# Optimization experiments

Hardware: AMD Instinct MI355X
Metric: run time of the kernel (lower is better)

Reference implementation:

```python
import jax, jax.numpy as jnp
import numpy as np

N = 50000       # nodes
E = 800000      # directed edges (before self-loops)
IN_C = 128
HID = 32
HEADS = 4
OUT_C = 64
NEG_SLOPE = 0.2  # PyG GATConv default leaky relu slope


def setup_inputs() -> dict:
    key = jax.random.key(0)
    ks = jax.random.split(key, 11)
    x = jax.random.normal(ks[0], (N, IN_C), jnp.float32)
    edge_index = jax.random.randint(ks[1], (2, E), 0, N, dtype=jnp.int32)
    # conv1: in -> HEADS*HID, concat=True
    W1 = jax.random.normal(ks[2], (IN_C, HEADS * HID), jnp.float32) / np.sqrt(IN_C)
    att_src1 = jax.random.normal(ks[3], (HEADS, HID), jnp.float32) / np.sqrt(HID)
    att_dst1 = jax.random.normal(ks[4], (HEADS, HID), jnp.float32) / np.sqrt(HID)
    b1 = jnp.zeros((HEADS * HID,), jnp.float32)
    # conv2: HEADS*HID -> OUT_C, heads=1, concat=False
    W2 = jax.random.normal(ks[5], (HEADS * HID, OUT_C), jnp.float32) / np.sqrt(HEADS * HID)
    att_src2 = jax.random.normal(ks[6], (1, OUT_C), jnp.float32) / np.sqrt(OUT_C)
    att_dst2 = jax.random.normal(ks[7], (1, OUT_C), jnp.float32) / np.sqrt(OUT_C)
    b2 = jnp.zeros((OUT_C,), jnp.float32)
    return dict(x=x, edge_index=edge_index, W1=W1, att_src1=att_src1,
                att_dst1=att_dst1, b1=b1, W2=W2, att_src2=att_src2,
                att_dst2=att_dst2, b2=b2)


def _gat_conv(x, src, dst, W, att_src, att_dst, bias, heads, ch, concat):
    # x: [N, F_in]; src/dst: [E'] (self-loops already included)
    h = (x @ W).reshape(N, heads, ch)                 # [N, H, C]
    a_s = jnp.sum(h * att_src[None], axis=-1)         # [N, H]
    a_d = jnp.sum(h * att_dst[None], axis=-1)         # [N, H]
    e = jax.nn.leaky_relu(a_s[src] + a_d[dst], NEG_SLOPE)  # [E', H]
    # numerically-stable edge softmax over destination neighborhoods
    m = jax.ops.segment_max(e, dst, num_segments=N)   # [N, H]
    m = jnp.where(jnp.isfinite(m), m, 0.0)
    ee = jnp.exp(e - jax.lax.stop_gradient(m)[dst])
    denom = jax.ops.segment_sum(ee, dst, num_segments=N)  # [N, H]
    alpha = ee / (denom[dst] + 1e-16)                 # [E', H]
    msg = h[src] * alpha[:, :, None]                  # [E', H, C]
    out = jax.ops.segment_sum(msg, dst, num_segments=N)   # [N, H, C]
    if concat:
        out = out.reshape(N, heads * ch)
    else:
        out = out.mean(axis=1)
    return out + bias


def reference(x, edge_index, W1, att_src1, att_dst1, b1, W2, att_src2, att_dst2, b2):
    # PyG GATConv adds self-loops by default
    loop = jnp.arange(N, dtype=edge_index.dtype)
    src = jnp.concatenate([edge_index[0], loop])
    dst = jnp.concatenate([edge_index[1], loop])
    # dropout layers are identity in eval mode (training=False)
    h = _gat_conv(x, src, dst, W1, att_src1, att_dst1, b1, HEADS, HID, True)
    h = jax.nn.elu(h)
    out = _gat_conv(h, src, dst, W2, att_src2, att_dst2, b2, 1, OUT_C, False)
    return out
```

## Files before the change

kernel.cpp:

```cpp
#include <hip/hip_runtime.h>
#include <math.h>

namespace {
constexpr int N_   = 50000;
constexpr int E_   = 800000;
constexpr int EP_  = E_ + N_;
constexpr float SLOPE = 0.2f;

constexpr int NB_    = (N_ + 127) / 128;
constexpr int CHUNK_ = 8192;
constexpr int NBLKA_ = (EP_ + CHUNK_ - 1) / CHUNK_;
constexpr int CAPB_  = 4096;
constexpr int NBLKG_ = (N_ + 63) / 64;

constexpr size_t OFF_H1  = 0;
constexpr size_t OFF_Y1  = OFF_H1  + (size_t)N_ * 128 * 2;
constexpr size_t OFF_H2  = OFF_Y1  + (size_t)N_ * 128 * 2;
constexpr size_t OFF_AS1 = OFF_H2  + (size_t)N_ * 64 * 2;
constexpr size_t OFF_AD1 = OFF_AS1 + (size_t)N_ * 4 * 4;
constexpr size_t OFF_AS2 = OFF_AD1 + (size_t)N_ * 4 * 4;
constexpr size_t OFF_AD2 = OFF_AS2 + (size_t)N_ * 4;
constexpr size_t OFF_ROW = OFF_AD2 + (size_t)N_ * 4;
constexpr size_t OFF_GC  = OFF_ROW + (((size_t)(N_ + 1) * 4 + 15) & ~(size_t)15);
constexpr size_t OFF_GO  = OFF_GC  + (((size_t)NB_ * 4 + 15) & ~(size_t)15);
constexpr size_t OFF_GU  = OFF_GO  + (((size_t)(NB_ + 1) * 4 + 15) & ~(size_t)15);
constexpr size_t OFF_EB1 = OFF_GU  + (((size_t)NB_ * 4 + 15) & ~(size_t)15);
constexpr size_t OFF_EB  = OFF_EB1 + (size_t)EP_ * 4;
}

typedef __attribute__((ext_vector_type(8))) short short8;
typedef __attribute__((ext_vector_type(4))) float f32x4;

__device__ __forceinline__ unsigned short f2bf(float x) {
  unsigned u = __float_as_uint(x);
  return (unsigned short)((u + 0x7FFFu + ((u >> 16) & 1u)) >> 16);
}
__device__ __forceinline__ unsigned pack2bf(float a, float b) {
  return (unsigned)f2bf(a) | ((unsigned)f2bf(b) << 16);
}
__device__ __forceinline__ float bf_lo(unsigned u) { return __uint_as_float(u << 16); }
__device__ __forceinline__ float bf_hi(unsigned u) { return __uint_as_float(u & 0xFFFF0000u); }

__global__ __launch_bounds__(256, 3) void k_g1h(const float* __restrict__ x,
    const float* __restrict__ W, const float* __restrict__ av_s,
    const float* __restrict__ av_d, unsigned short* __restrict__ hbf,
    float* __restrict__ a_s, float* __restrict__ a_d,
    const int* __restrict__ ei, int* __restrict__ gcount)
{
  __shared__ __align__(16) char smem[52224];
  const int t = threadIdx.x;
  if (blockIdx.x >= NBLKG_) {
    int* nh = (int*)smem;
    for (int j = t; j < NB_; j += 256) nh[j] = 0;
    __syncthreads();
    const int beg = (blockIdx.x - NBLKG_) * CHUNK_;
    const int end = min(beg + CHUNK_, EP_);
    for (int i = beg + t; i < end; i += 256) {
      const int dd = (i < E_) ? ei[E_ + i] : (i - E_);
      atomicAdd(&nh[dd >> 7], 1);
    }
    __syncthreads();
    for (int j = t; j < NB_; j += 256)
      if (nh[j]) atomicAdd(&gcount[j], nh[j]);
    return;
  }
  unsigned short* xs = (unsigned short*)smem;
  unsigned*       wt = (unsigned*)(smem + 17408);
  float*         wtf = (float*)(smem + 17408);
  const int rbase = blockIdx.x * 64;
#pragma unroll
  for (int it = 0; it < 8; ++it) {
    const int fidx = t + it * 256;
    const int row = fidx >> 5;
    const int c4  = fidx & 31;
    const int rg  = rbase + row;
    float4 v = (rg < N_) ? ((const float4*)x)[(size_t)rg * 32 + c4]
                         : make_float4(0.f, 0.f, 0.f, 0.f);
    *(uint2*)&xs[row * 136 + c4 * 4] =
        make_uint2(pack2bf(v.x, v.y), pack2bf(v.z, v.w));
  }
#pragma unroll
  for (int it = 0; it < 32; ++it) {
    const int idx = t + it * 256;
    const int n  = idx & 127;
    const int kk = idx >> 7;
    wt[n * 68 + kk] = pack2bf(W[(2 * kk) * 128 + n], W[(2 * kk + 1) * 128 + n]);
  }
  __syncthreads();
  const int wv = t >> 6;
  const int l  = t & 63;
  const int lr = l & 15;
  const int lg = l >> 4;
  f32x4 acc[8];
#pragma unroll
  for (int j = 0; j < 8; ++j) acc[j] = (f32x4){0.f, 0.f, 0.f, 0.f};
#pragma unroll
  for (int ks = 0; ks < 4; ++ks) {
    const short8 a = *(const short8*)&xs[(wv * 16 + lr) * 136 + ks * 32 + lg * 8];
#pragma unroll
    for (int j = 0; j < 8; ++j) {
      const short8 b = *(const short8*)&wt[(j * 16 + lr) * 68 + ks * 16 + lg * 4];
      acc[j] = __builtin_amdgcn_mfma_f32_16x16x32_bf16(a, b, acc[j], 0, 0, 0);
    }
  }
  __syncthreads();
#pragma unroll
  for (int j = 0; j < 8; ++j)
#pragma unroll
    for (int r = 0; r < 4; ++r)
      wtf[(wv * 16 + lg * 4 + r) * 132 + j * 16 + lr] = acc[j][r];
  __syncthreads();
#pragma unroll
  for (int it = 0; it < 16; ++it) {
    const int idx = t + it * 256;
    const int row = idx >> 6;
    const int c2  = idx & 63;
    const int rg  = rbase + row;
    if (rg < N_) {
      const float2 hv = *(const float2*)&wtf[row * 132 + c2 * 2];
      ((unsigned*)hbf)[(size_t)rg * 64 + c2] = pack2bf(hv.x, hv.y);
    }
  }
  {
    const int row = t & 63;
    const int q   = t >> 6;
    const int rg  = rbase + row;
    float ss = 0.f, sd = 0.f;
#pragma unroll
    for (int i = 0; i < 8; ++i) {
      const float4 hv = *(const float4*)&wtf[row * 132 + q * 32 + 4 * i];
      const float4 s4 = *(const float4*)&av_s[q * 32 + 4 * i];
      const float4 d4 = *(const float4*)&av_d[q * 32 + 4 * i];
      ss += hv.x * s4.x + hv.y * s4.y + hv.z * s4.z + hv.w * s4.w;
      sd += hv.x * d4.x + hv.y * d4.y + hv.z * d4.z + hv.w * d4.w;
    }
    if (rg < N_) { a_s[rg * 4 + q] = ss; a_d[rg * 4 + q] = sd; }
  }
}

__global__ __launch_bounds__(256, 4) void k_gemm2(const unsigned* __restrict__ ybf,
    const float* __restrict__ W, const float* __restrict__ av_s,
    const float* __restrict__ av_d, unsigned short* __restrict__ hbf,
    float* __restrict__ a_s, float* __restrict__ a_d)
{
  __shared__ __align__(16) char smem[36864];
  unsigned short* xs = (unsigned short*)smem;
  unsigned*       wt = (unsigned*)(smem + 17408);
  float*         wtf = (float*)(smem + 17408);
  float*          ps = (float*)(smem + 34816);
  const int t = threadIdx.x;
  const int rbase = blockIdx.x * 64;
#pragma unroll
  for (int it = 0; it < 16; ++it) {
    const int idx = t + it * 256;
    const int row = idx >> 6;
    const int c2  = idx & 63;
    const int rg  = rbase + row;
    const unsigned u = (rg < N_) ? ybf[(size_t)rg * 64 + c2] : 0u;
    *(unsigned*)&xs[row * 136 + c2 * 2] = u;
  }
#pragma unroll
  for (int it = 0; it < 16; ++it) {
    const int idx = t + it * 256;
    const int n  = idx & 63;
    const int kk = idx >> 6;
    wt[n * 68 + kk] = pack2bf(W[(2 * kk) * 64 + n], W[(2 * kk + 1) * 64 + n]);
  }
  __syncthreads();
  const int wv = t >> 6;
  const int l  = t & 63;
  const int lr = l & 15;
  const int lg = l >> 4;
  f32x4 acc[4];
#pragma unroll
  for (int j = 0; j < 4; ++j) acc[j] = (f32x4){0.f, 0.f, 0.f, 0.f};
#pragma unroll
  for (int ks = 0; ks < 4; ++ks) {
    const short8 a = *(const short8*)&xs[(wv * 16 + lr) * 136 + ks * 32 + lg * 8];
#pragma unroll
    for (int j = 0; j < 4; ++j) {
      const short8 b = *(const short8*)&wt[(j * 16 + lr) * 68 + ks * 16 + lg * 4];
      acc[j] = __builtin_amdgcn_mfma_f32_16x16x32_bf16(a, b, acc[j], 0, 0, 0);
    }
  }
  __syncthreads();
#pragma unroll
  for (int j = 0; j < 4; ++j)
#pragma unroll
    for (int r = 0; r < 4; ++r)
      wtf[(wv * 16 + lg * 4 + r) * 68 + j * 16 + lr] = acc[j][r];
  __syncthreads();
#pragma unroll
  for (int it = 0; it < 8; ++it) {
    const int idx = t + it * 256;
    const int row = idx >> 5;
    const int c2  = idx & 31;
    const int rg  = rbase + row;
    if (rg < N_) {
      const float2 hv = *(const float2*)&wtf[row * 68 + c2 * 2];
      ((unsigned*)hbf)[(size_t)rg * 32 + c2] = pack2bf(hv.x, hv.y);
    }
  }
  {
    const int row = t & 63;
    const int g   = t >> 6;
    float ss = 0.f, sd = 0.f;
#pragma unroll
    for (int i = 0; i < 4; ++i) {
      const float4 hv = *(const float4*)&wtf[row * 68 + g * 16 + 4 * i];
      const float4 s4 = *(const float4*)&av_s[g * 16 + 4 * i];
      const float4 d4 = *(const float4*)&av_d[g * 16 + 4 * i];
      ss += hv.x * s4.x + hv.y * s4.y + hv.z * s4.z + hv.w * s4.w;
      sd += hv.x * d4.x + hv.y * d4.y + hv.z * d4.z + hv.w * d4.w;
    }
    ps[g * 64 + row] = ss;
    ps[256 + g * 64 + row] = sd;
  }
  __syncthreads();
  if (t < 64) {
    const int rg = rbase + t;
    if (rg < N_) {
      a_s[rg] = ps[t] + ps[64 + t] + ps[128 + t] + ps[192 + t];
      a_d[rg] = ps[256 + t] + ps[320 + t] + ps[384 + t] + ps[448 + t];
    }
  }
}

__global__ __launch_bounds__(512) void k_scan(const int* __restrict__ gcount,
    int* __restrict__ goff, int* __restrict__ gcursor)
{
  __shared__ int sd[512];
  const int t = threadIdx.x;
  const int v = (t < NB_) ? gcount[t] : 0;
  sd[t] = v;
  __syncthreads();
  for (int off = 1; off < 512; off <<= 1) {
    const int add = (t >= off) ? sd[t - off] : 0;
    __syncthreads();
    sd[t] += add;
    __syncthreads();
  }
  if (t < NB_) { goff[t] = sd[t] - v; gcursor[t] = sd[t] - v; }
  if (t == 0) goff[NB_] = EP_;
}

__global__ __launch_bounds__(256) void k_scatter(const int* __restrict__ ei,
    int* __restrict__ gcursor, unsigned* __restrict__ eb1)
{
  __shared__ int nh[NB_];
  __shared__ int gb[NB_];
  const int t = threadIdx.x;
  for (int j = t; j < NB_; j += 256) nh[j] = 0;
  __syncthreads();
  const int beg = blockIdx.x * CHUNK_;
  const int end = min(beg + CHUNK_, EP_);
  for (int i = beg + t; i < end; i += 256) {
    const int d = (i < E_) ? ei[E_ + i] : (i - E_);
    atomicAdd(&nh[d >> 7], 1);
  }
  __syncthreads();
  for (int j = t; j < NB_; j += 256) {
    const int c = nh[j];
    gb[j] = c ? atomicAdd(&gcursor[j], c) : 0;
    nh[j] = 0;
  }
  __syncthreads();
  for (int i = beg + t; i < end; i += 256) {
    int s, d;
    if (i < E_) { s = ei[i]; d = ei[E_ + i]; } else { s = d = i - E_; }
    const int b = d >> 7;
    const int r = atomicAdd(&nh[b], 1);
    eb1[gb[b] + r] = ((unsigned)s << 16) | (unsigned)d;
  }
}

__global__ __launch_bounds__(256) void k_bucket(const unsigned* __restrict__ eb1,
    const int* __restrict__ goff, int* __restrict__ rowptr,
    int* __restrict__ ebuf)
{
  __shared__ int h[128];
  __shared__ int off[129];
  __shared__ unsigned arrv[CAPB_];
  const int b = blockIdx.x;
  const int t = threadIdx.x;
  const int base = goff[b];
  const int cnt  = goff[b + 1] - base;
  if (t < 128) h[t] = 0;
  __syncthreads();
  const bool fits = (cnt <= CAPB_);
  for (int i = t; i < cnt; i += 256) {
    const unsigned v = eb1[base + i];
    if (fits) arrv[i] = v;
    atomicAdd(&h[(int)(v & 0xFFFFu) - (b << 7)], 1);
  }
  __syncthreads();
  if (t < 64) {
    const int a0 = h[2 * t], a1 = h[2 * t + 1];
    int s = a0 + a1;
#pragma unroll
    for (int m = 1; m < 64; m <<= 1) {
      const int u = __shfl_up(s, m);
      if (t >= m) s += u;
    }
    off[2 * t + 1] = s - a1;
    off[2 * t]     = s - a1 - a0;
    if (t == 63) off[128] = s;
  }
  __syncthreads();
  if (t < 128) {
    const int dst = (b << 7) + t;
    if (dst < N_) rowptr[dst] = base + off[t];
  }
  if (b == NB_ - 1 && t == 0) rowptr[N_] = EP_;
  if (t < 128) h[t] = 0;
  __syncthreads();
  for (int i = t; i < cnt; i += 256) {
    const unsigned v = fits ? arrv[i] : eb1[base + i];
    const int dlow = (int)(v & 0xFFFFu) - (b << 7);
    const int r = atomicAdd(&h[dlow], 1);
    ebuf[base + off[dlow] + r] = (int)(v >> 16);
  }
}

__global__ __launch_bounds__(256, 4) void k_agg1(const int* __restrict__ rowptr,
    const int* __restrict__ ebuf, const float* __restrict__ a_s,
    const float* __restrict__ a_d, const unsigned short* __restrict__ hbf,
    const float* __restrict__ b1, unsigned* __restrict__ y)
{
  __shared__ uint2 pl[4][4 * 65];
  const int w = threadIdx.x >> 6;
  const int l = threadIdx.x & 63;
  const int d = blockIdx.x * 2 + (w >> 1);
  const int half = w & 1;
  const int base = rowptr[d];
  const int deg  = rowptr[d + 1] - base;
  const float4 ad = *(const float4*)&a_d[(size_t)d * 4];
  const int pe = l >> 5;
  const int ci = half * 32 + (l & 31);
  const int hsel = ci >> 4;
  const unsigned ci4 = (unsigned)ci * 4u;
  float acc0 = 0.f, acc1 = 0.f;
  float r0, r1, r2, r3;

  if (deg <= 64) {
    int   sreg = 0;
    float e0 = -1e30f, e1 = -1e30f, e2 = -1e30f, e3 = -1e30f;
    if (l < deg) {
      sreg = ebuf[base + l];
      const float4 as = *(const float4*)&a_s[(size_t)sreg * 4];
      e0 = as.x + ad.x; e0 = e0 > 0.f ? e0 : SLOPE * e0;
      e1 = as.y + ad.y; e1 = e1 > 0.f ? e1 : SLOPE * e1;
      e2 = as.z + ad.z; e2 = e2 > 0.f ? e2 : SLOPE * e2;
      e3 = as.w + ad.w; e3 = e3 > 0.f ? e3 : SLOPE * e3;
    }
    float mx0 = e0, mx1 = e1, mx2 = e2, mx3 = e3;
#pragma unroll
    for (int m = 32; m >= 1; m >>= 1) {
      mx0 = fmaxf(mx0, __shfl_xor(mx0, m));
      mx1 = fmaxf(mx1, __shfl_xor(mx1, m));
      mx2 = fmaxf(mx2, __shfl_xor(mx2, m));
      mx3 = fmaxf(mx3, __shfl_xor(mx3, m));
    }
    const float p0 = (l < deg) ? __expf(e0 - mx0) : 0.f;
    const float p1 = (l < deg) ? __expf(e1 - mx1) : 0.f;
    const float p2 = (l < deg) ? __expf(e2 - mx2) : 0.f;
    const float p3 = (l < deg) ? __expf(e3 - mx3) : 0.f;
    float sm0 = p0, sm1 = p1, sm2 = p2, sm3 = p3;
#pragma unroll
    for (int m = 32; m >= 1; m >>= 1) {
      sm0 += __shfl_xor(sm0, m);
      sm1 += __shfl_xor(sm1, m);
      sm2 += __shfl_xor(sm2, m);
      sm3 += __shfl_xor(sm3, m);
    }
    r0 = 1.f / (sm0 + 1e-16f);
    r1 = 1.f / (sm1 + 1e-16f);
    r2 = 1.f / (sm2 + 1e-16f);
    r3 = 1.f / (sm3 + 1e-16f);
    {
      const unsigned soff = (unsigned)sreg << 8;
      pl[w][0 * 65 + l] = make_uint2(soff, __float_as_uint(p0));
      pl[w][1 * 65 + l] = make_uint2(soff, __float_as_uint(p1));
      pl[w][2 * 65 + l] = make_uint2(soff, __float_as_uint(p2));
      pl[w][3 * 65 + l] = make_uint2(soff, __float_as_uint(p3));
    }
    const uint2* __restrict__ rp = &pl[w][hsel * 65 + pe];
    const int niter = (deg + 15) >> 4;
    int it = 0;
    for (; it + 2 <= niter; it += 2) {
      unsigned uA[8], uB[8];
      float pA[8], pB[8];
#pragma unroll
      for (int u = 0; u < 8; ++u) {
        const uint2 sp = rp[it * 16 + 2 * u];
        pA[u] = __uint_as_float(sp.y);
        uA[u] = *(const unsigned*)((const char*)hbf + (sp.x + ci4));
      }
#pragma unroll
      for (int u = 0; u < 8; ++u) {
        const uint2 sp = rp[it * 16 + 16 + 2 * u];
        pB[u] = __uint_as_float(sp.y);
        uB[u] = *(const unsigned*)((const char*)hbf + (sp.x + ci4));
      }
#pragma unroll
      for (int u = 0; u < 8; ++u) {
        acc0 = fmaf(pA[u], bf_lo(uA[u]), acc0);
        acc1 = fmaf(pA[u], bf_hi(uA[u]), acc1);
      }
#pragma unroll
      for (int u = 0; u < 8; ++u) {
        acc0 = fmaf(pB[u], bf_lo(uB[u]), acc0);
        acc1 = fmaf(pB[u], bf_hi(uB[u]), acc1);
      }
    }
    if (it < niter) {
      unsigned uA[8];
      float pA[8];
#pragma unroll
      for (int u = 0; u < 8; ++u) {
        const uint2 sp = rp[it * 16 + 2 * u];
        pA[u] = __uint_as_float(sp.y);
        uA[u] = *(const unsigned*)((const char*)hbf + (sp.x + ci4));
      }
#pragma unroll
      for (int u = 0; u < 8; ++u) {
        acc0 = fmaf(pA[u], bf_lo(uA[u]), acc0);
        acc1 = fmaf(pA[u], bf_hi(uA[u]), acc1);
      }
    }
  } else {
    float mx0 = -1e30f, mx1 = -1e30f, mx2 = -1e30f, mx3 = -1e30f;
    for (int i = l; i < deg; i += 64) {
      const int s = ebuf[base + i];
      const float4 as = *(const float4*)&a_s[(size_t)s * 4];
      float e0 = as.x + ad.x; e0 = e0 > 0.f ? e0 : SLOPE * e0;
      float e1 = as.y + ad.y; e1 = e1 > 0.f ? e1 : SLOPE * e1;
      float e2 = as.z + ad.z; e2 = e2 > 0.f ? e2 : SLOPE * e2;
      float e3 = as.w + ad.w; e3 = e3 > 0.f ? e3 : SLOPE * e3;
      mx0 = fmaxf(mx0, e0); mx1 = fmaxf(mx1, e1);
      mx2 = fmaxf(mx2, e2); mx3 = fmaxf(mx3, e3);
    }
#pragma unroll
    for (int m = 32; m >= 1; m >>= 1) {
      mx0 = fmaxf(mx0, __shfl_xor(mx0, m));
      mx1 = fmaxf(mx1, __shfl_xor(mx1, m));
      mx2 = fmaxf(mx2, __shfl_xor(mx2, m));
      mx3 = fmaxf(mx3, __shfl_xor(mx3, m));
    }
    float sm0 = 0.f, sm1 = 0.f, sm2 = 0.f, sm3 = 0.f;
    for (int i = l; i < deg; i += 64) {
      const int s = ebuf[base + i];
      const float4 as = *(const float4*)&a_s[(size_t)s * 4];
      float e0 = as.x + ad.x; e0 = e0 > 0.f ? e0 : SLOPE * e0;
      float e1 = as.y + ad.y; e1 = e1 > 0.f ? e1 : SLOPE * e1;
      float e2 = as.z + ad.z; e2 = e2 > 0.f ? e2 : SLOPE * e2;
      float e3 = as.w + ad.w; e3 = e3 > 0.f ? e3 : SLOPE * e3;
      sm0 += __expf(e0 - mx0); sm1 += __expf(e1 - mx1);
      sm2 += __expf(e2 - mx2); sm3 += __expf(e3 - mx3);
    }
#pragma unroll
    for (int m = 32; m >= 1; m >>= 1) {
      sm0 += __shfl_xor(sm0, m);
      sm1 += __shfl_xor(sm1, m);
      sm2 += __shfl_xor(sm2, m);
      sm3 += __shfl_xor(sm3, m);
    }
    r0 = 1.f / (sm0 + 1e-16f);
    r1 = 1.f / (sm1 + 1e-16f);
    r2 = 1.f / (sm2 + 1e-16f);
    r3 = 1.f / (sm3 + 1e-16f);
    const float mxs = hsel == 3 ? mx3 : hsel == 2 ? mx2 : hsel == 1 ? mx1 : mx0;
    for (int i = 0; i < deg; i += 2) {
      const int e = i + pe;
      if (e < deg) {
        const int s = ebuf[base + e];
        const float4 as = *(const float4*)&a_s[(size_t)s * 4];
        float e0 = as.x + ad.x; e0 = e0 > 0.f ? e0 : SLOPE * e0;
        float e1 = as.y + ad.y; e1 = e1 > 0.f ? e1 : SLOPE * e1;
        float e2 = as.z + ad.z; e2 = e2 > 0.f ? e2 : SLOPE * e2;
        float e3 = as.w + ad.w; e3 = e3 > 0.f ? e3 : SLOPE * e3;
        const float es = hsel == 3 ? e3 : hsel == 2 ? e2 : hsel == 1 ? e1 : e0;
        const float pa = __expf(es - mxs);
        const unsigned uu = ((const unsigned*)(hbf + (size_t)s * 128))[ci];
        acc0 = fmaf(pa, bf_lo(uu), acc0);
        acc1 = fmaf(pa, bf_hi(uu), acc1);
      }
    }
  }
  acc0 += __shfl_xor(acc0, 32);
  acc1 += __shfl_xor(acc1, 32);
  if (pe == 0) {
    const float rsel = hsel == 3 ? r3 : hsel == 2 ? r2 : hsel == 1 ? r1 : r0;
    const int c0 = 2 * ci;
    const float2 bb = *(const float2*)&b1[c0];
    float o0 = acc0 * rsel + bb.x;
    float o1 = acc1 * rsel + bb.y;
    o0 = o0 > 0.f ? o0 : expm1f(o0);
    o1 = o1 > 0.f ? o1 : expm1f(o1);
    y[(size_t)d * 64 + ci] = pack2bf(o0, o1);
  }
}

__global__ __launch_bounds__(256, 4) void k_agg2(const int* __restrict__ rowptr,
    const int* __restrict__ ebuf, const float* __restrict__ a_s,
    const float* __restrict__ a_d, const unsigned short* __restrict__ hbf,
    const float* __restrict__ b2, float* __restrict__ out)
{
  __shared__ uint2 pl2[4][66];
  const int w = threadIdx.x >> 6;
  const int l = threadIdx.x & 63;
  const int lh = l & 31;
  const bool hi = (l >= 32);
  const int d = blockIdx.x * 4 + w;
  const int base = rowptr[d];
  const int deg  = rowptr[d + 1] - base;
  const float ad = a_d[d];
  const unsigned lh4 = (unsigned)lh * 4u;
  float acc0 = 0.f, acc1 = 0.f;
  float rv;

  if (deg <= 64) {
    int   sreg = 0;
    float e = -1e30f;
    if (l < deg) {
      sreg = ebuf[base + l];
      e = a_s[sreg] + ad; e = e > 0.f ? e : SLOPE * e;
    }
    float mx = e;
#pragma unroll
    for (int m = 32; m >= 1; m >>= 1) mx = fmaxf(mx, __shfl_xor(mx, m));
    const float p = (l < deg) ? __expf(e - mx) : 0.f;
    float sm = p;
#pragma unroll
    for (int m = 32; m >= 1; m >>= 1) sm += __shfl_xor(sm, m);
    rv = 1.f / (sm + 1e-16f);
    pl2[w][l] = make_uint2((unsigned)(l < deg ? sreg : 0) << 7,
                           __float_as_uint(p));
    const uint2* __restrict__ rp = &pl2[w][hi ? 1 : 0];
    const int niter = (deg + 15) >> 4;
    int it = 0;
    for (; it + 2 <= niter; it += 2) {
      unsigned uA[8], uB[8];
      float pA[8], pB[8];
#pragma unroll
      for (int u = 0; u < 8; ++u) {
        const uint2 sp = rp[it * 16 + 2 * u];
        pA[u] = __uint_as_float(sp.y);
        uA[u] = *(const unsigned*)((const char*)hbf + (sp.x + lh4));
      }
#pragma unroll
      for (int u = 0; u < 8; ++u) {
        const uint2 sp = rp[it * 16 + 16 + 2 * u];
        pB[u] = __uint_as_float(sp.y);
        uB[u] = *(const unsigned*)((const char*)hbf + (sp.x + lh4));
      }
#pragma unroll
      for (int u = 0; u < 8; ++u) {
        acc0 = fmaf(pA[u], bf_lo(uA[u]), acc0);
        acc1 = fmaf(pA[u], bf_hi(uA[u]), acc1);
      }
#pragma unroll
      for (int u = 0; u < 8; ++u) {
        acc0 = fmaf(pB[u], bf_lo(uB[u]), acc0);
        acc1 = fmaf(pB[u], bf_hi(uB[u]), acc1);
      }
    }
    if (it < niter) {
      unsigned uA[8];
      float pA[8];
#pragma unroll
      for (int u = 0; u < 8; ++u) {
        const uint2 sp = rp[it * 16 + 2 * u];
        pA[u] = __uint_as_float(sp.y);
        uA[u] = *(const unsigned*)((const char*)hbf + (sp.x + lh4));
      }
#pragma unroll
      for (int u = 0; u < 8; ++u) {
        acc0 = fmaf(pA[u], bf_lo(uA[u]), acc0);
        acc1 = fmaf(pA[u], bf_hi(uA[u]), acc1);
      }
    }
  } else {
    float mx = -1e30f;
    for (int i = l; i < deg; i += 64) {
      const int s = ebuf[base + i];
      float e = a_s[s] + ad; e = e > 0.f ? e : SLOPE * e;
      mx = fmaxf(mx, e);
    }
#pragma unroll
    for (int m = 32; m >= 1; m >>= 1) mx = fmaxf(mx, __shfl_xor(mx, m));
    float sm = 0.f;
    for (int i = l; i < deg; i += 64) {
      const int s = ebuf[base + i];
      float e = a_s[s] + ad; e = e > 0.f ? e : SLOPE * e;
      sm += __expf(e - mx);
    }
#pragma unroll
    for (int m = 32; m >= 1; m >>= 1) sm += __shfl_xor(sm, m);
    rv = 1.f / (sm + 1e-16f);
    for (int i = 0; i < deg; ++i) {
      const int s = ebuf[base + i];
      float e = a_s[s] + ad; e = e > 0.f ? e : SLOPE * e;
      const float pp = hi ? 0.f : __expf(e - mx);
      const unsigned uu = ((const unsigned*)(hbf + (size_t)s * 64))[lh];
      acc0 = fmaf(pp, bf_lo(uu), acc0);
      acc1 = fmaf(pp, bf_hi(uu), acc1);
    }
  }
  acc0 += __shfl_xor(acc0, 32);
  acc1 += __shfl_xor(acc1, 32);
  if (!hi) {
    const int c0 = 2 * lh;
    const float2 bb = *(const float2*)&b2[c0];
    *(float2*)&out[(size_t)d * 64 + c0] =
        make_float2(acc0 * rv + bb.x, acc1 * rv + bb.y);
  }
}

extern "C" void kernel_launch(void* const* d_in, const int* in_sizes, int n_in,
                              void* d_out, int out_size, void* d_ws, size_t ws_size,
                              hipStream_t stream) {
  const float* x     = (const float*)d_in[0];
  const int*   ei    = (const int*)d_in[1];
  const float* W1    = (const float*)d_in[2];
  const float* as1v  = (const float*)d_in[3];
  const float* ad1v  = (const float*)d_in[4];
  const float* b1    = (const float*)d_in[5];
  const float* W2    = (const float*)d_in[6];
  const float* as2v  = (const float*)d_in[7];
  const float* ad2v  = (const float*)d_in[8];
  const float* b2    = (const float*)d_in[9];
  float* out = (float*)d_out;

  char* ws = (char*)d_ws;
  unsigned short* h1 = (unsigned short*)(ws + OFF_H1);
  unsigned* y1       = (unsigned*)(ws + OFF_Y1);
  unsigned short* h2 = (unsigned short*)(ws + OFF_H2);
  float* a_s1 = (float*)(ws + OFF_AS1);
  float* a_d1 = (float*)(ws + OFF_AD1);
  float* a_s2 = (float*)(ws + OFF_AS2);
  float* a_d2 = (float*)(ws + OFF_AD2);
  int* rowptr = (int*)(ws + OFF_ROW);
  int* gcount = (int*)(ws + OFF_GC);
  int* goff   = (int*)(ws + OFF_GO);
  int* gcur   = (int*)(ws + OFF_GU);
  unsigned* eb1 = (unsigned*)(ws + OFF_EB1);
  int* ebuf   = (int*)(ws + OFF_EB);

  hipMemsetAsync(gcount, 0, (size_t)NB_ * 4, stream);

  k_g1h<<<NBLKG_ + NBLKA_, 256, 0, stream>>>(x, W1, as1v, ad1v, h1, a_s1, a_d1,
                                             ei, gcount);
  k_scan<<<1, 512, 0, stream>>>(gcount, goff, gcur);
  k_scatter<<<NBLKA_, 256, 0, stream>>>(ei, gcur, eb1);
  k_bucket<<<NB_, 256, 0, stream>>>(eb1, goff, rowptr, ebuf);
  k_agg1<<<N_ / 2, 256, 0, stream>>>(rowptr, ebuf, a_s1, a_d1, h1, b1, y1);
  k_gemm2<<<NBLKG_, 256, 0, stream>>>(y1, W2, as2v, ad2v, h2, a_s2, a_d2);
  k_agg2<<<N_ / 4, 256, 0, stream>>>(rowptr, ebuf, a_s2, a_d2, h2, b2, out);
}
```

Baseline: 178.9 us.

## Map one wavefront per node in aggregation kernels with 8-byte bf16 gathers

k_agg1 now assigns one full wavefront per destination node instead of two wavefronts per node. Each lane gathers 4 bf16 channels (uint2) per neighbor, so two edge slots cover the 128-channel row. k_agg2 likewise uses uint2 gathers over 16 lanes with four edges in flight, finishing with two shuffle reductions. The aim is to halve duplicated softmax work and wave count in agg1 and widen memory transactions, at the cost of more registers and fewer lanes per node for the gather.

```diff
diff --git a/kernel.cpp b/kernel.cpp
--- a/kernel.cpp
+++ b/kernel.cpp
@@ -330,17 +330,10 @@
   __shared__ uint2 pl[4][4 * 65];
   const int w = threadIdx.x >> 6;
   const int l = threadIdx.x & 63;
-  const int d = blockIdx.x * 2 + (w >> 1);
-  const int half = w & 1;
+  const int d = blockIdx.x * 4 + w;
   const int base = rowptr[d];
   const int deg  = rowptr[d + 1] - base;
   const float4 ad = *(const float4*)&a_d[(size_t)d * 4];
-  const int pe = l >> 5;
-  const int ci = half * 32 + (l & 31);
-  const int hsel = ci >> 4;
-  const unsigned ci4 = (unsigned)ci * 4u;
-  float acc0 = 0.f, acc1 = 0.f;
-  float r0, r1, r2, r3;
 
   if (deg <= 64) {
     int   sreg = 0;
@@ -373,10 +366,10 @@
       sm2 += __shfl_xor(sm2, m);
       sm3 += __shfl_xor(sm3, m);
     }
-    r0 = 1.f / (sm0 + 1e-16f);
-    r1 = 1.f / (sm1 + 1e-16f);
-    r2 = 1.f / (sm2 + 1e-16f);
-    r3 = 1.f / (sm3 + 1e-16f);
+    const float r0 = 1.f / (sm0 + 1e-16f);
+    const float r1 = 1.f / (sm1 + 1e-16f);
+    const float r2 = 1.f / (sm2 + 1e-16f);
+    const float r3 = 1.f / (sm3 + 1e-16f);
     {
       const unsigned soff = (unsigned)sreg << 8;
       pl[w][0 * 65 + l] = make_uint2(soff, __float_as_uint(p0));
@@ -384,51 +377,81 @@
       pl[w][2 * 65 + l] = make_uint2(soff, __float_as_uint(p2));
       pl[w][3 * 65 + l] = make_uint2(soff, __float_as_uint(p3));
     }
-    const uint2* __restrict__ rp = &pl[w][hsel * 65 + pe];
+    const int eh = l >> 5;
+    const int cl = l & 31;
+    const int hsel = cl >> 3;
+    const unsigned coff = (unsigned)cl * 8u;
+    const uint2* __restrict__ rp = &pl[w][hsel * 65];
+    float acc0 = 0.f, acc1 = 0.f, acc2 = 0.f, acc3 = 0.f;
     const int niter = (deg + 15) >> 4;
-    int it = 0;
-    for (; it + 2 <= niter; it += 2) {
-      unsigned uA[8], uB[8];
+    int bt = 0;
+    for (; bt + 2 <= niter; bt += 2) {
+      uint2 uA[8], uB[8];
       float pA[8], pB[8];
 #pragma unroll
       for (int u = 0; u < 8; ++u) {
-        const uint2 sp = rp[it * 16 + 2 * u];
+        const uint2 sp = rp[bt * 16 + 2 * u + eh];
         pA[u] = __uint_as_float(sp.y);
-        uA[u] = *(const unsigned*)((const char*)hbf + (sp.x + ci4));
-      }
-#pragma unroll
-      for (int u = 0; u < 8; ++u) {
-        const uint2 sp = rp[it * 16 + 16 + 2 * u];
+        uA[u] = *(const uint2*)((const char*)hbf + (sp.x + coff));
+      }
+#pragma unroll
+      for (int u = 0; u < 8; ++u) {
+        const uint2 sp = rp[bt * 16 + 16 + 2 * u + eh];
         pB[u] = __uint_as_float(sp.y);
-        uB[u] = *(const unsigned*)((const char*)hbf + (sp.x + ci4));
-      }
-#pragma unroll
-      for (int u = 0; u < 8; ++u) {
-        acc0 = fmaf(pA[u], bf_lo(uA[u]), acc0);
-        acc1 = fmaf(pA[u], bf_hi(uA[u]), acc1);
-      }
-#pragma unroll
-      for (int u = 0; u < 8; ++u) {
-        acc0 = fmaf(pB[u], bf_lo(uB[u]), acc0);
-        acc1 = fmaf(pB[u], bf_hi(uB[u]), acc1);
-      }
-    }
-    if (it < niter) {
-      unsigned uA[8];
+        uB[u] = *(const uint2*)((const char*)hbf + (sp.x + coff));
+      }
+#pragma unroll
+      for (int u = 0; u < 8; ++u) {
+        acc0 = fmaf(pA[u], bf_lo(uA[u].x), acc0);
+        acc1 = fmaf(pA[u], bf_hi(uA[u].x), acc1);
+        acc2 = fmaf(pA[u], bf_lo(uA[u].y), acc2);
+        acc3 = fmaf(pA[u], bf_hi(uA[u].y), acc3);
+      }
+#pragma unroll
+      for (int u = 0; u < 8; ++u) {
+        acc0 = fmaf(pB[u], bf_lo(uB[u].x), acc0);
+        acc1 = fmaf(pB[u], bf_hi(uB[u].x), acc1);
+        acc2 = fmaf(pB[u], bf_lo(uB[u].y), acc2);
+        acc3 = fmaf(pB[u], bf_hi(uB[u].y), acc3);
+      }
+    }
+    if (bt < niter) {
+      uint2 uA[8];
       float pA[8];
 #pragma unroll
       for (int u = 0; u < 8; ++u) {
-        const uint2 sp = rp[it * 16 + 2 * u];
+        const uint2 sp = rp[bt * 16 + 2 * u + eh];
         pA[u] = __uint_as_float(sp.y);
-        uA[u] = *(const unsigned*)((const char*)hbf + (sp.x + ci4));
-      }
-#pragma unroll
-      for (int u = 0; u < 8; ++u) {
-        acc0 = fmaf(pA[u], bf_lo(uA[u]), acc0);
-        acc1 = fmaf(pA[u], bf_hi(uA[u]), acc1);
-      }
+        uA[u] = *(const uint2*)((const char*)hbf + (sp.x + coff));
+      }
+#pragma unroll
+      for (int u = 0; u < 8; ++u) {
+        acc0 = fmaf(pA[u], bf_lo(uA[u].x), acc0);
+        acc1 = fmaf(pA[u], bf_hi(uA[u].x), acc1);
+        acc2 = fmaf(pA[u], bf_lo(uA[u].y), acc2);
+        acc3 = fmaf(pA[u], bf_hi(uA[u].y), acc3);
+      }
+    }
+    acc0 += __shfl_xor(acc0, 32);
+    acc1 += __shfl_xor(acc1, 32);
+    acc2 += __shfl_xor(acc2, 32);
+    acc3 += __shfl_xor(acc3, 32);
+    if (eh == 0) {
+      const float rsel = hsel == 3 ? r3 : hsel == 2 ? r2 : hsel == 1 ? r1 : r0;
+      const float4 bb = *(const float4*)&b1[4 * cl];
+      float o0 = acc0 * rsel + bb.x;
+      float o1 = acc1 * rsel + bb.y;
+      float o2 = acc2 * rsel + bb.z;
+      float o3 = acc3 * rsel + bb.w;
+      o0 = o0 > 0.f ? o0 : expm1f(o0);
+      o1 = o1 > 0.f ? o1 : expm1f(o1);
+      o2 = o2 > 0.f ? o2 : expm1f(o2);
+      o3 = o3 > 0.f ? o3 : expm1f(o3);
+      *(uint2*)&y[(size_t)d * 64 + 2 * cl] =
+          make_uint2(pack2bf(o0, o1), pack2bf(o2, o3));
     }
   } else {
+    const int hsel = l >> 4;
     float mx0 = -1e30f, mx1 = -1e30f, mx2 = -1e30f, mx3 = -1e30f;
     for (int i = l; i < deg; i += 64) {
       const int s = ebuf[base + i];
@@ -465,39 +488,32 @@
       sm2 += __shfl_xor(sm2, m);
       sm3 += __shfl_xor(sm3, m);
     }
-    r0 = 1.f / (sm0 + 1e-16f);
-    r1 = 1.f / (sm1 + 1e-16f);
-    r2 = 1.f / (sm2 + 1e-16f);
-    r3 = 1.f / (sm3 + 1e-16f);
+    const float r0 = 1.f / (sm0 + 1e-16f);
+    const float r1 = 1.f / (sm1 + 1e-16f);
+    const float r2 = 1.f / (sm2 + 1e-16f);
+    const float r3 = 1.f / (sm3 + 1e-16f);
     const float mxs = hsel == 3 ? mx3 : hsel == 2 ? mx2 : hsel == 1 ? mx1 : mx0;
-    for (int i = 0; i < deg; i += 2) {
-      const int e = i + pe;
-      if (e < deg) {
-        const int s = ebuf[base + e];
-        const float4 as = *(const float4*)&a_s[(size_t)s * 4];
-        float e0 = as.x + ad.x; e0 = e0 > 0.f ? e0 : SLOPE * e0;
-        float e1 = as.y + ad.y; e1 = e1 > 0.f ? e1 : SLOPE * e1;
-        float e2 = as.z + ad.z; e2 = e2 > 0.f ? e2 : SLOPE * e2;
-        float e3 = as.w + ad.w; e3 = e3 > 0.f ? e3 : SLOPE * e3;
-        const float es = hsel == 3 ? e3 : hsel == 2 ? e2 : hsel == 1 ? e1 : e0;
-        const float pa = __expf(es - mxs);
-        const unsigned uu = ((const unsigned*)(hbf + (size_t)s * 128))[ci];
-        acc0 = fmaf(pa, bf_lo(uu), acc0);
-        acc1 = fmaf(pa, bf_hi(uu), acc1);
-      }
-    }
-  }
-  acc0 += __shfl_xor(acc0, 32);
-  acc1 += __shfl_xor(acc1, 32);
-  if (pe == 0) {
+    float acc0 = 0.f, acc1 = 0.f;
+    for (int i = 0; i < deg; ++i) {
+      const int s = ebuf[base + i];
+      const float4 as = *(const float4*)&a_s[(size_t)s * 4];
+      float e0 = as.x + ad.x; e0 = e0 > 0.f ? e0 : SLOPE * e0;
+      float e1 = as.y + ad.y; e1 = e1 > 0.f ? e1 : SLOPE * e1;
+      float e2 = as.z + ad.z; e2 = e2 > 0.f ? e2 : SLOPE * e2;
+      float e3 = as.w + ad.w; e3 = e3 > 0.f ? e3 : SLOPE * e3;
+      const float es = hsel == 3 ? e3 : hsel == 2 ? e2 : hsel == 1 ? e1 : e0;
+      const float pa = __expf(es - mxs);
+      const unsigned uu = ((const unsigned*)(hbf + (size_t)s * 128))[l];
+      acc0 = fmaf(pa, bf_lo(uu), acc0);
+      acc1 = fmaf(pa, bf_hi(uu), acc1);
+    }
     const float rsel = hsel == 3 ? r3 : hsel == 2 ? r2 : hsel == 1 ? r1 : r0;
-    const int c0 = 2 * ci;
-    const float2 bb = *(const float2*)&b1[c0];
+    const float2 bb = *(const float2*)&b1[2 * l];
     float o0 = acc0 * rsel + bb.x;
     float o1 = acc1 * rsel + bb.y;
     o0 = o0 > 0.f ? o0 : expm1f(o0);
     o1 = o1 > 0.f ? o1 : expm1f(o1);
-    y[(size_t)d * 64 + ci] = pack2bf(o0, o1);
+    y[(size_t)d * 64 + l] = pack2bf(o0, o1);
   }
 }
 
@@ -509,15 +525,10 @@
   __shared__ uint2 pl2[4][66];
   const int w = threadIdx.x >> 6;
   const int l = threadIdx.x & 63;
-  const int lh = l & 31;
-  const bool hi = (l >= 32);
   const int d = blockIdx.x * 4 + w;
   const int base = rowptr[d];
   const int deg  = rowptr[d + 1] - base;
   const float ad = a_d[d];
-  const unsigned lh4 = (unsigned)lh * 4u;
-  float acc0 = 0.f, acc1 = 0.f;
-  float rv;
 
   if (deg <= 64) {
     int   sreg = 0;
@@ -533,54 +544,80 @@
     float sm = p;
 #pragma unroll
     for (int m = 32; m >= 1; m >>= 1) sm += __shfl_xor(sm, m);
-    rv = 1.f / (sm + 1e-16f);
+    const float rv = 1.f / (sm + 1e-16f);
     pl2[w][l] = make_uint2((unsigned)(l < deg ? sreg : 0) << 7,
                            __float_as_uint(p));
-    const uint2* __restrict__ rp = &pl2[w][hi ? 1 : 0];
-    const int niter = (deg + 15) >> 4;
-    int it = 0;
-    for (; it + 2 <= niter; it += 2) {
-      unsigned uA[8], uB[8];
+    const int eq = l >> 4;
+    const int cl = l & 15;
+    const unsigned coff = (unsigned)cl * 8u;
+    const uint2* __restrict__ rp = &pl2[w][0];
+    float acc0 = 0.f, acc1 = 0.f, acc2 = 0.f, acc3 = 0.f;
+    const int niter = (deg + 31) >> 5;
+    int bt = 0;
+    for (; bt + 2 <= niter; bt += 2) {
+      uint2 uA[8], uB[8];
       float pA[8], pB[8];
 #pragma unroll
       for (int u = 0; u < 8; ++u) {
-        const uint2 sp = rp[it * 16 + 2 * u];
+        const uint2 sp = rp[bt * 32 + 4 * u + eq];
         pA[u] = __uint_as_float(sp.y);
-        uA[u] = *(const unsigned*)((const char*)hbf + (sp.x + lh4));
-      }
-#pragma unroll
-      for (int u = 0; u < 8; ++u) {
-        const uint2 sp = rp[it * 16 + 16 + 2 * u];
+        uA[u] = *(const uint2*)((const char*)hbf + (sp.x + coff));
+      }
+#pragma unroll
+      for (int u = 0; u < 8; ++u) {
+        const uint2 sp = rp[bt * 32 + 32 + 4 * u + eq];
         pB[u] = __uint_as_float(sp.y);
-        uB[u] = *(const unsigned*)((const char*)hbf + (sp.x + lh4));
-      }
-#pragma unroll
-      for (int u = 0; u < 8; ++u) {
-        acc0 = fmaf(pA[u], bf_lo(uA[u]), acc0);
-        acc1 = fmaf(pA[u], bf_hi(uA[u]), acc1);
-      }
-#pragma unroll
-      for (int u = 0; u < 8; ++u) {
-        acc0 = fmaf(pB[u], bf_lo(uB[u]), acc0);
-        acc1 = fmaf(pB[u], bf_hi(uB[u]), acc1);
-      }
-    }
-    if (it < niter) {
-      unsigned uA[8];
+        uB[u] = *(const uint2*)((const char*)hbf + (sp.x + coff));
+      }
+#pragma unroll
+      for (int u = 0; u < 8; ++u) {
+        acc0 = fmaf(pA[u], bf_lo(uA[u].x), acc0);
+        acc1 = fmaf(pA[u], bf_hi(uA[u].x), acc1);
+        acc2 = fmaf(pA[u], bf_lo(uA[u].y), acc2);
+        acc3 = fmaf(pA[u], bf_hi(uA[u].y), acc3);
+      }
+#pragma unroll
+      for (int u = 0; u < 8; ++u) {
+        acc0 = fmaf(pB[u], bf_lo(uB[u].x), acc0);
+        acc1 = fmaf(pB[u], bf_hi(uB[u].x), acc1);
+        acc2 = fmaf(pB[u], bf_lo(uB[u].y), acc2);
+        acc3 = fmaf(pB[u], bf_hi(uB[u].y), acc3);
+      }
+    }
+    if (bt < niter) {
+      uint2 uA[8];
       float pA[8];
 #pragma unroll
       for (int u = 0; u < 8; ++u) {
-        const uint2 sp = rp[it * 16 + 2 * u];
+        const uint2 sp = rp[bt * 32 + 4 * u + eq];
         pA[u] = __uint_as_float(sp.y);
-        uA[u] = *(const unsigned*)((const char*)hbf + (sp.x + lh4));
-      }
-#pragma unroll
-      for (int u = 0; u < 8; ++u) {
-        acc0 = fmaf(pA[u], bf_lo(uA[u]), acc0);
-        acc1 = fmaf(pA[u], bf_hi(uA[u]), acc1);
-      }
+        uA[u] = *(const uint2*)((const char*)hbf + (sp.x + coff));
+      }
+#pragma unroll
+      for (int u = 0; u < 8; ++u) {
+        acc0 = fmaf(pA[u], bf_lo(uA[u].x), acc0);
+        acc1 = fmaf(pA[u], bf_hi(uA[u].x), acc1);
+        acc2 = fmaf(pA[u], bf_lo(uA[u].y), acc2);
+        acc3 = fmaf(pA[u], bf_hi(uA[u].y), acc3);
+      }
+    }
+    acc0 += __shfl_xor(acc0, 32);
+    acc1 += __shfl_xor(acc1, 32);
+    acc2 += __shfl_xor(acc2, 32);
+    acc3 += __shfl_xor(acc3, 32);
+    acc0 += __shfl_xor(acc0, 16);
+    acc1 += __shfl_xor(acc1, 16);
+    acc2 += __shfl_xor(acc2, 16);
+    acc3 += __shfl_xor(acc3, 16);
+    if (eq == 0) {
+      const float4 bb = *(const float4*)&b2[4 * cl];
+      *(float4*)&out[(size_t)d * 64 + 4 * cl] =
+          make_float4(acc0 * rv + bb.x, acc1 * rv + bb.y,
+                      acc2 * rv + bb.z, acc3 * rv + bb.w);
     }
   } else {
+    const int lh = l & 31;
+    const bool hi = (l >= 32);
     float mx = -1e30f;
     for (int i = l; i < deg; i += 64) {
       const int s = ebuf[base + i];
@@ -597,7 +634,8 @@
     }
 #pragma unroll
     for (int m = 32; m >= 1; m >>= 1) sm += __shfl_xor(sm, m);
-    rv = 1.f / (sm + 1e-16f);
+    const float rv = 1.f / (sm + 1e-16f);
+    float acc0 = 0.f, acc1 = 0.f;
     for (int i = 0; i < deg; ++i) {
       const int s = ebuf[base + i];
       float e = a_s[s] + ad; e = e > 0.f ? e : SLOPE * e;
@@ -606,14 +644,14 @@
       acc0 = fmaf(pp, bf_lo(uu), acc0);
       acc1 = fmaf(pp, bf_hi(uu), acc1);
     }
-  }
-  acc0 += __shfl_xor(acc0, 32);
-  acc1 += __shfl_xor(acc1, 32);
-  if (!hi) {
-    const int c0 = 2 * lh;
-    const float2 bb = *(const float2*)&b2[c0];
-    *(float2*)&out[(size_t)d * 64 + c0] =
-        make_float2(acc0 * rv + bb.x, acc1 * rv + bb.y);
+    acc0 += __shfl_xor(acc0, 32);
+    acc1 += __shfl_xor(acc1, 32);
+    if (!hi) {
+      const int c0 = 2 * lh;
+      const float2 bb = *(const float2*)&b2[c0];
+      *(float2*)&out[(size_t)d * 64 + c0] =
+          make_float2(acc0 * rv + bb.x, acc1 * rv + bb.y);
+    }
   }
 }
 
@@ -654,7 +692,7 @@
   k_scan<<<1, 512, 0, stream>>>(gcount, goff, gcur);
   k_scatter<<<NBLKA_, 256, 0, stream>>>(ei, gcur, eb1);
   k_bucket<<<NB_, 256, 0, stream>>>(eb1, goff, rowptr, ebuf);
-  k_agg1<<<N_ / 2, 256, 0, stream>>>(rowptr, ebuf, a_s1, a_d1, h1, b1, y1);
+  k_agg1<<<N_ / 4, 256, 0, stream>>>(rowptr, ebuf, a_s1, a_d1, h1, b1, y1);
   k_gemm2<<<NBLKG_, 256, 0, stream>>>(y1, W2, as2v, ad2v, h2, a_s2, a_d2);
   k_agg2<<<N_ / 4, 256, 0, stream>>>(rowptr, ebuf, a_s2, a_d2, h2, b2, out);
 }
```

Result: faster. 167.1 us (-6.6%).
